# Optimization experiments

Hardware: AMD Instinct MI355X
Metric: run time of the kernel (lower is better)

Reference implementation:

```python
import jax, jax.numpy as jnp
import numpy as np

HEADS = 16
KEY_SIZE = 64
HEAD_SIZE = 64
D_MODEL = 1024
MASK_BIG = 1e12


def setup_inputs() -> dict:
    key = jax.random.key(0)
    ks = jax.random.split(key, 16)
    B, S, D = 4, 2048, D_MODEL
    qk_dim = HEADS * KEY_SIZE
    out_dim = HEADS * HEAD_SIZE
    s = 0.02
    return {
        'q': jax.random.normal(ks[0], (B, S, D), jnp.float32),
        'k': jax.random.normal(ks[1], (B, S, D), jnp.float32),
        'v': jax.random.normal(ks[2], (B, S, D), jnp.float32),
        'q_mask': jax.random.randint(ks[3], (B, S), 0, 2, jnp.int32),
        'v_mask': jax.random.randint(ks[4], (B, S), 0, 2, jnp.int32),
        'Wq': jax.random.normal(ks[5], (D, qk_dim), jnp.float32) * s,
        'bq': jnp.zeros((qk_dim,), jnp.float32),
        'Wk': jax.random.normal(ks[6], (D, qk_dim), jnp.float32) * s,
        'bk': jnp.zeros((qk_dim,), jnp.float32),
        'Wv': jax.random.normal(ks[7], (D, out_dim), jnp.float32) * s,
        'bv': jnp.zeros((out_dim,), jnp.float32),
        'Wo': jax.random.normal(ks[8], (out_dim, out_dim), jnp.float32) * s,
        'bo': jnp.zeros((out_dim,), jnp.float32),
    }


def reference(q, k, v, q_mask, v_mask, Wq, bq, Wk, bk, Wv, bv, Wo, bo):
    B, Sq, _ = q.shape
    Sk = k.shape[1]
    # projections -> [B, H, S, d]
    qw = (q @ Wq + bq).reshape(B, Sq, HEADS, KEY_SIZE).transpose(0, 2, 1, 3)
    kw = (k @ Wk + bk).reshape(B, Sk, HEADS, KEY_SIZE).transpose(0, 2, 1, 3)
    vw = (v @ Wv + bv).reshape(B, Sk, HEADS, HEAD_SIZE).transpose(0, 2, 1, 3)
    # scaled dot-product scores [B, H, Sq, Sk]
    a = jnp.einsum('bhqd,bhkd->bhqk', qw, kw) / np.sqrt(KEY_SIZE).astype(np.float32)
    # v_mask: additive -inf-like penalty on padded keys (mode=1, axis=-1)
    vm = v_mask.astype(a.dtype)[:, None, None, :]
    a = a - (1.0 - vm) * MASK_BIG
    # a_mask=True: causal mask (mask future positions)
    causal = jnp.tril(jnp.ones((Sq, Sk), a.dtype))
    a = a - (1.0 - causal) * MASK_BIG
    a = jax.nn.softmax(a, axis=-1)
    # attention output [B, Sq, H*head_size]
    o = jnp.einsum('bhqk,bhkd->bhqd', a, vw).transpose(0, 2, 1, 3).reshape(B, Sq, HEADS * HEAD_SIZE)
    o = o @ Wo + bo
    # q_mask: multiplicative zeroing of padded query outputs (mode=0, axis=1)
    o = o * q_mask.astype(o.dtype)[:, :, None]
    return o
```

## Files before the change

kernel.cpp:

```cpp
#include <hip/hip_runtime.h>
#include <hip/hip_bf16.h>

typedef __attribute__((ext_vector_type(8))) short v8s;
typedef __attribute__((ext_vector_type(4))) float v4f;
typedef __attribute__((ext_vector_type(16))) float v16f;
typedef __attribute__((ext_vector_type(4))) unsigned v4u;

#define S_LEN 2048
#define NB 4
#define NH 16
#define LOG2E 1.4426950408889634f
#define CMASK 1443109011456.0f
#define DEFER_THR 11.55f

__device__ __forceinline__ short f2bf(float f) {
    __hip_bfloat16 h = __float2bfloat16(f);
    union { __hip_bfloat16 h; short s; } u; u.h = h; return u.s;
}

__device__ __forceinline__ unsigned cvtpk(float lo, float hi) {
    unsigned r;
    asm("v_cvt_pk_bf16_f32 %0, %1, %2" : "=v"(r) : "v"(lo), "v"(hi));
    return r;
}

__device__ __forceinline__ int swz(int row, int col) {
    return (row * 128 + col) ^ ((row & 7) << 4);
}

__device__ __forceinline__ void async16(void* lds, const void* g) {
    __builtin_amdgcn_global_load_lds(
        (const __attribute__((address_space(1))) unsigned int*)g,
        (__attribute__((address_space(3))) unsigned int*)lds, 16, 0, 0);
}

#define MFMA16(a, b, c) __builtin_amdgcn_mfma_f32_16x16x32_bf16((a), (b), (c), 0, 0, 0)
#define MFMA32(a, b, c) __builtin_amdgcn_mfma_f32_32x32x16_bf16((a), (b), (c), 0, 0, 0)

__global__ __launch_bounds__(256) void convert_all(const float* __restrict__ q,
                                                   const float* __restrict__ k,
                                                   const float* __restrict__ v,
                                                   short* __restrict__ Xq,
                                                   short* __restrict__ Xk,
                                                   short* __restrict__ Xv,
                                                   float* __restrict__ outz) {
    if (blockIdx.y == 3) {
        size_t i = ((size_t)blockIdx.x * 256 + threadIdx.x) * 8;
        float4 z4 = {0.f, 0.f, 0.f, 0.f};
        *(float4*)(outz + i) = z4;
        *(float4*)(outz + i + 4) = z4;
        return;
    }
    const float* in = (blockIdx.y == 0) ? q : (blockIdx.y == 1) ? k : v;
    short* out = (blockIdx.y == 0) ? Xq : (blockIdx.y == 1) ? Xk : Xv;
    size_t i = ((size_t)blockIdx.x * 256 + threadIdx.x) * 8;
    float4 a = *(const float4*)(in + i);
    float4 b = *(const float4*)(in + i + 4);
    v8s o;
    o[0] = f2bf(a.x); o[1] = f2bf(a.y); o[2] = f2bf(a.z); o[3] = f2bf(a.w);
    o[4] = f2bf(b.x); o[5] = f2bf(b.y); o[6] = f2bf(b.z); o[7] = f2bf(b.w);
    *(v8s*)(out + i) = o;
}

__global__ __launch_bounds__(256) void build_pen(const int* __restrict__ vm,
                                                 short* __restrict__ penC) {
    int i = blockIdx.x * 256 + threadIdx.x;
    penC[i] = vm[i] ? (short)0 : f2bf(-CMASK);
}

__global__ __launch_bounds__(256) void compact_qmask(const int* __restrict__ qm,
                                                     int* __restrict__ idx,
                                                     int* __restrict__ nq) {
    const int b = blockIdx.x;
    const int* m = qm + b * S_LEN;
    int* ib = idx + b * S_LEN;
    __shared__ int cnt[256];
    const int t = threadIdx.x;
    int loc[8], c = 0;
#pragma unroll
    for (int i = 0; i < 8; ++i) { int s = t * 8 + i; if (m[s]) loc[c++] = s; }
    cnt[t] = c;
    __syncthreads();
    for (int d = 1; d < 256; d <<= 1) {
        int v = (t >= d) ? cnt[t - d] : 0;
        __syncthreads();
        cnt[t] += v;
        __syncthreads();
    }
    int off = cnt[t] - c;
    for (int i = 0; i < c; ++i) ib[off + i] = loc[i];
    if (t == 255) nq[b] = cnt[255];
}

__global__ __launch_bounds__(256) void transpose_all(const float* __restrict__ Wq,
                                                     const float* __restrict__ Wk,
                                                     const float* __restrict__ Wv,
                                                     const float* __restrict__ Wo,
                                                     short* __restrict__ WTq,
                                                     short* __restrict__ WTk,
                                                     short* __restrict__ WTv,
                                                     short* __restrict__ WTo) {
    const int z = blockIdx.z;
    const float* W = (z == 0) ? Wq : (z == 1) ? Wk : (z == 2) ? Wv : Wo;
    short* WT = (z == 0) ? WTq : (z == 1) ? WTk : (z == 2) ? WTv : WTo;
    __shared__ float tile[32][33];
    int k0 = blockIdx.x * 32, n0 = blockIdx.y * 32;
    int tx = threadIdx.x & 31, ty = threadIdx.x >> 5;
#pragma unroll
    for (int i = 0; i < 4; ++i)
        tile[ty + i * 8][tx] = W[(size_t)(k0 + ty + i * 8) * 1024 + n0 + tx];
    __syncthreads();
#pragma unroll
    for (int i = 0; i < 4; ++i)
        WT[(size_t)(n0 + ty + i * 8) * 1024 + k0 + tx] = f2bf(tile[tx][ty + i * 8]);
}

__global__ __launch_bounds__(256)
void proj_all(const short* __restrict__ Xk, const short* __restrict__ Xv,
              const short* __restrict__ Xq,
              const short* __restrict__ WTk, const short* __restrict__ WTv,
              const short* __restrict__ WTq,
              const float* __restrict__ bk, const float* __restrict__ bv,
              const float* __restrict__ bq,
              const int* __restrict__ idx, const int* __restrict__ nq,
              short* __restrict__ KF, short* __restrict__ VF,
              short* __restrict__ QW) {
    __shared__ short As[2][128 * 64];
    __shared__ short Bs[2][128 * 64];
    const int tid = threadIdx.x;
    const int l = tid & 63, w = tid >> 6;
    const int g = l >> 4, ql = l & 15;
    const int z = blockIdx.z;
    const int bid = blockIdx.x;
    const int y = (bid & 7) + 8 * (bid >> 6);
    const int n0 = ((bid >> 3) & 7) * 128;
    const int wr = w >> 1, wc = w & 1;

    int b = 0, m0 = y * 128, m0c = 0, nqv = 0;
    const int* idxb = nullptr;
    if (z == 2) {
        if (y >= 36) return;
        b = y / 9; m0c = (y % 9) * 128;
        nqv = nq[b];
        if (m0c >= nqv) return;
        idxb = idx + b * S_LEN;
    }
    const short* A  = (z == 0) ? Xk : (z == 1) ? Xv : Xq;
    const short* BT = (z == 0) ? WTk : (z == 1) ? WTv : WTq;
    const float* bias = (z == 0) ? bk : (z == 1) ? bv : bq;

    int arow[4];
#pragma unroll
    for (int i = 0; i < 4; ++i) {
        int row = (i * 256 + tid) >> 3;
        if (z == 2) {
            int jc = m0c + row;
            arow[i] = b * S_LEN + idxb[(jc < nqv) ? jc : (nqv - 1)];
        } else {
            arow[i] = m0 + row;
        }
    }
    const int c8 = (((l & 7) ^ (l >> 3))) * 8;

    v4f acc[4][4] = {};

    auto stage = [&](int kt, int buf) {
        const int kk = kt * 64;
#pragma unroll
        for (int i = 0; i < 4; ++i) {
            int ci = i * 256 + tid;
            async16((char*)As[buf] + (size_t)(i * 256 + w * 64) * 16,
                    A + (size_t)arow[i] * 1024 + kk + c8);
            async16((char*)Bs[buf] + (size_t)(i * 256 + w * 64) * 16,
                    BT + (size_t)(n0 + (ci >> 3)) * 1024 + kk + c8);
        }
    };

    stage(0, 0);
    for (int kt = 0; kt < 16; ++kt) {
        __builtin_amdgcn_s_barrier();
        __builtin_amdgcn_sched_barrier(0);
        if (kt + 1 < 16) {
            stage(kt + 1, (kt + 1) & 1);
            asm volatile("s_waitcnt vmcnt(8)" ::: "memory");
        } else {
            asm volatile("s_waitcnt vmcnt(0)" ::: "memory");
        }
        __builtin_amdgcn_sched_barrier(0);
        __builtin_amdgcn_s_barrier();
        __builtin_amdgcn_sched_barrier(0);
        const short* Ab = As[kt & 1];
        const short* Bb = Bs[kt & 1];
#pragma unroll
        for (int ks = 0; ks < 2; ++ks) {
            v8s af[4], bfr[4];
#pragma unroll
            for (int mt = 0; mt < 4; ++mt)
                af[mt] = *(const v8s*)((char*)Ab +
                          swz(wr * 64 + mt * 16 + ql, ks * 64 + g * 16));
#pragma unroll
            for (int nt = 0; nt < 4; ++nt)
                bfr[nt] = *(const v8s*)((char*)Bb +
                          swz(wc * 64 + nt * 16 + ql, ks * 64 + g * 16));
#pragma unroll
            for (int mt = 0; mt < 4; ++mt)
#pragma unroll
                for (int nt = 0; nt < 4; ++nt)
                    acc[mt][nt] = MFMA16(af[mt], bfr[nt], acc[mt][nt]);
        }
    }

#pragma unroll
    for (int nt = 0; nt < 4; ++nt) {
        int col = n0 + wc * 64 + nt * 16 + ql;
        float bval = bias[col];
        int hh = col >> 6, dd = col & 63;
#pragma unroll
        for (int mt = 0; mt < 4; ++mt) {
#pragma unroll
            for (int r = 0; r < 4; ++r) {
                int lrow = wr * 64 + mt * 16 + g * 4 + r;
                float vv = acc[mt][nt][r] + bval;
                if (z == 0) {
                    int gm = m0 + lrow;
                    int bb = gm >> 11, ss = gm & 2047;
                    size_t base = (size_t)(bb * NH + hh) * 131072
                                + (size_t)(ss >> 6) * 4096
                                + (dd >> 4) * 1024 + (ss & 63) * 16
                                + ((dd >> 3) & 1) * 8 + (dd & 7);
                    KF[base] = f2bf(vv);
                } else if (z == 1) {
                    int gm = m0 + lrow;
                    int bb = gm >> 11, ss = gm & 2047;
                    int wkp = ss & 63;
                    size_t base = (size_t)(bb * NH + hh) * 131072
                                + (size_t)(ss >> 6) * 4096
                                + (wkp >> 4) * 1024 + dd * 16
                                + ((wkp >> 3) & 1) * 8 + (wkp & 7);
                    VF[base] = f2bf(vv);
                } else {
                    int jc = m0c + lrow;
                    vv *= 0.125f * LOG2E;
                    QW[((size_t)(b * NH + hh) * S_LEN + jc) * 64 + dd] = f2bf(vv);
                }
            }
        }
    }
}

__global__ __launch_bounds__(64)
void attn_kernel(const short* __restrict__ QW, const short* __restrict__ KF,
                 const short* __restrict__ VF, const short* __restrict__ penC,
                 const int* __restrict__ idx, const int* __restrict__ nq,
                 short* __restrict__ O) {
    const int l = threadIdx.x;
    const int lq = l & 31, hi = l >> 5;
    const int bh = blockIdx.x;
    const int chunk = 63 - (int)blockIdx.y;
    const int b = bh >> 4, hd = bh & 15;

    const int nqv = nq[b];
    const int cy = chunk * 32;
    if (cy >= nqv) return;

    const short* Qp = QW + (size_t)bh * S_LEN * 64;
    const short* Kp = KF + (size_t)bh * 131072;
    const short* Vp = VF + (size_t)bh * 131072;
    const short* pp = penC + b * S_LEN;
    const int* idxb = idx + b * S_LEN;

    const int j = cy + lq;
    const int jj = (j < nqv) ? j : (nqv - 1);
    const int q_glob = idxb[jj];
    const int qmin = __builtin_amdgcn_readfirstlane(q_glob);

    int lastj = cy + 31; if (lastj > nqv - 1) lastj = nqv - 1;
    const int NT = (idxb[lastj] >> 6) + 1;

    v8s qf[4];
#pragma unroll
    for (int ks = 0; ks < 4; ++ks)
        qf[ks] = *(const v8s*)(Qp + (size_t)jj * 64 + ks * 16 + hi * 8);
    v8s qf4 = {};
    qf4[0] = hi ? (short)0 : (short)0x3F80;

    v16f accO[2] = {};
    float m_run = -INFINITY, l_run = 0.f;

    auto tile = [&](int kt, bool causal) {
        const int k0 = kt * 64;
        const short* Kt = Kp + (size_t)kt * 4096;
        const short* Vt = Vp + (size_t)kt * 4096;
        short p0 = pp[k0 + lq], p1 = pp[k0 + lq + 32];

        v8s kf0[4], kf1[4];
#pragma unroll
        for (int ks = 0; ks < 4; ++ks) {
            kf0[ks] = *(const v8s*)(Kt + ks * 1024 + lq * 16 + hi * 8);
            kf1[ks] = *(const v8s*)(Kt + ks * 1024 + (lq + 32) * 16 + hi * 8);
        }
        v16f acc0 = {}, acc1 = {};
        __builtin_amdgcn_s_setprio(1);
#pragma unroll
        for (int ks = 0; ks < 4; ++ks) {
            acc0 = MFMA32(kf0[ks], qf[ks], acc0);
            acc1 = MFMA32(kf1[ks], qf[ks], acc1);
        }
        v8s k4a = {}, k4b = {};
        k4a[0] = hi ? (short)0 : p0;
        k4b[0] = hi ? (short)0 : p1;
        acc0 = MFMA32(k4a, qf4, acc0);
        acc1 = MFMA32(k4b, qf4, acc1);
        __builtin_amdgcn_s_setprio(0);

        float s[32];
#pragma unroll
        for (int jn = 0; jn < 16; ++jn) { s[jn] = acc0[jn]; s[16 + jn] = acc1[jn]; }
        if (causal) {
#pragma unroll
            for (int t = 0; t < 2; ++t)
#pragma unroll
                for (int jn = 0; jn < 16; ++jn) {
                    int kp = k0 + t * 32 + (jn & 3) + 8 * (jn >> 2) + 4 * hi;
                    if (kp > q_glob) s[t * 16 + jn] -= CMASK;
                }
        }
        float t8[8];
#pragma unroll
        for (int i = 0; i < 8; ++i)
            t8[i] = fmaxf(fmaxf(s[i], s[i + 8]), fmaxf(s[i + 16], s[i + 24]));
#pragma unroll
        for (int i = 0; i < 4; ++i) t8[i] = fmaxf(t8[i], t8[i + 4]);
        float tmax = fmaxf(fmaxf(t8[0], t8[1]), fmaxf(t8[2], t8[3]));
        tmax = fmaxf(tmax, __shfl_xor(tmax, 32, 64));

        if (__any(tmax > m_run + DEFER_THR)) {
            float mnew = fmaxf(m_run, tmax);
            float scale = exp2f(m_run - mnew);
            m_run = mnew;
            l_run *= scale;
#pragma unroll
            for (int jn = 0; jn < 16; ++jn) {
                float sc = __shfl(scale, (jn & 3) + 8 * (jn >> 2) + 4 * hi, 64);
                accO[0][jn] *= sc;
                accO[1][jn] *= sc;
            }
        }
#pragma unroll
        for (int i = 0; i < 32; ++i) s[i] = exp2f(s[i] - m_run);
        float u8[8];
#pragma unroll
        for (int i = 0; i < 8; ++i)
            u8[i] = (s[i] + s[i + 8]) + (s[i + 16] + s[i + 24]);
#pragma unroll
        for (int i = 0; i < 4; ++i) u8[i] += u8[i + 4];
        float psum = (u8[0] + u8[1]) + (u8[2] + u8[3]);
        psum += __shfl_xor(psum, 32, 64);
        l_run += psum;

        v8s vf0[4], vf1[4];
#pragma unroll
        for (int ks = 0; ks < 4; ++ks) {
            vf0[ks] = *(const v8s*)(Vt + ks * 1024 + lq * 16 + hi * 8);
            vf1[ks] = *(const v8s*)(Vt + ks * 1024 + (lq + 32) * 16 + hi * 8);
        }

        v8s PA[4];
#pragma unroll
        for (int t = 0; t < 2; ++t)
#pragma unroll
            for (int sf = 0; sf < 2; ++sf) {
                int base = t * 16 + sf * 8;
                unsigned x0 = cvtpk(s[base + 0], s[base + 1]);
                unsigned x1 = cvtpk(s[base + 2], s[base + 3]);
                unsigned y0 = cvtpk(s[base + 4], s[base + 5]);
                unsigned y1 = cvtpk(s[base + 6], s[base + 7]);
                asm volatile("v_permlane32_swap_b32 %0, %1" : "+v"(x0), "+v"(y0));
                asm volatile("v_permlane32_swap_b32 %0, %1" : "+v"(x1), "+v"(y1));
                v4u wv; wv[0] = x0; wv[1] = x1; wv[2] = y0; wv[3] = y1;
                union { v4u u; v8s s8; } cvt; cvt.u = wv;
                PA[t * 2 + sf] = cvt.s8;
            }

        __builtin_amdgcn_s_setprio(1);
#pragma unroll
        for (int ks = 0; ks < 4; ++ks) {
            accO[0] = MFMA32(PA[ks], vf0[ks], accO[0]);
            accO[1] = MFMA32(PA[ks], vf1[ks], accO[1]);
        }
        __builtin_amdgcn_s_setprio(0);
    };

    for (int kt = 0; kt < NT; ++kt)
        tile(kt, kt * 64 + 63 > qmin);

    int kt = NT;
    while (kt < 32 && __any(m_run < -1e11f)) {
        tile(kt, true);
        ++kt;
    }

    float inv = 1.0f / l_run;
#pragma unroll
    for (int jn = 0; jn < 16; ++jn) {
        int rowq = (jn & 3) + 8 * (jn >> 2) + 4 * hi;
        float iv = __shfl(inv, rowq, 64);
        int jrow = cy + rowq;
        if (jrow < nqv) {
            size_t base = (size_t)(b * S_LEN + jrow) * 1024 + hd * 64 + lq;
            O[base]      = f2bf(accO[0][jn] * iv);
            O[base + 32] = f2bf(accO[1][jn] * iv);
        }
    }
}

__global__ __launch_bounds__(256)
void out_gemm_c(const short* __restrict__ A, const short* __restrict__ BT,
                const float* __restrict__ bias, const int* __restrict__ idx,
                const int* __restrict__ nq, float* __restrict__ out) {
    __shared__ short As[2][128 * 64];
    __shared__ short Bs[2][128 * 64];
    const int tid = threadIdx.x;
    const int l = tid & 63, w = tid >> 6;
    const int g = l >> 4, ql = l & 15;
    const int bid = blockIdx.x;
    const int y = (bid & 7) + 8 * (bid >> 6);
    if (y >= 36) return;
    const int n0 = ((bid >> 3) & 7) * 128;
    const int b = y / 9;
    const int m0c = (y % 9) * 128;
    const int nqv = nq[b];
    if (m0c >= nqv) return;
    const int* idxb = idx + b * S_LEN;
    const int wr = w >> 1, wc = w & 1;
    const int c8 = (((l & 7) ^ (l >> 3))) * 8;

    v4f acc[4][4] = {};

    auto stage = [&](int kt, int buf) {
        const int kk = kt * 64;
#pragma unroll
        for (int i = 0; i < 4; ++i) {
            int ci = i * 256 + tid;
            int row = ci >> 3;
            async16((char*)As[buf] + (size_t)(i * 256 + w * 64) * 16,
                    A + (size_t)(b * S_LEN + m0c + row) * 1024 + kk + c8);
            async16((char*)Bs[buf] + (size_t)(i * 256 + w * 64) * 16,
                    BT + (size_t)(n0 + row) * 1024 + kk + c8);
        }
    };

    stage(0, 0);
    for (int kt = 0; kt < 16; ++kt) {
        __builtin_amdgcn_s_barrier();
        __builtin_amdgcn_sched_barrier(0);
        if (kt + 1 < 16) {
            stage(kt + 1, (kt + 1) & 1);
            asm volatile("s_waitcnt vmcnt(8)" ::: "memory");
        } else {
            asm volatile("s_waitcnt vmcnt(0)" ::: "memory");
        }
        __builtin_amdgcn_sched_barrier(0);
        __builtin_amdgcn_s_barrier();
        __builtin_amdgcn_sched_barrier(0);
        const short* Ab = As[kt & 1];
        const short* Bb = Bs[kt & 1];
#pragma unroll
        for (int ks = 0; ks < 2; ++ks) {
            v8s af[4], bfr[4];
#pragma unroll
            for (int mt = 0; mt < 4; ++mt)
                af[mt] = *(const v8s*)((char*)Ab +
                          swz(wr * 64 + mt * 16 + ql, ks * 64 + g * 16));
#pragma unroll
            for (int nt = 0; nt < 4; ++nt)
                bfr[nt] = *(const v8s*)((char*)Bb +
                          swz(wc * 64 + nt * 16 + ql, ks * 64 + g * 16));
#pragma unroll
            for (int mt = 0; mt < 4; ++mt)
#pragma unroll
                for (int nt = 0; nt < 4; ++nt)
                    acc[mt][nt] = MFMA16(af[mt], bfr[nt], acc[mt][nt]);
        }
    }

#pragma unroll
    for (int nt = 0; nt < 4; ++nt) {
        int col = n0 + wc * 64 + nt * 16 + ql;
        float bval = bias[col];
#pragma unroll
        for (int mt = 0; mt < 4; ++mt) {
#pragma unroll
            for (int r = 0; r < 4; ++r) {
                int jc = m0c + wr * 64 + mt * 16 + g * 4 + r;
                if (jc < nqv) {
                    int orig = idxb[jc];
                    out[(size_t)(b * S_LEN + orig) * 1024 + col] =
                        acc[mt][nt][r] + bval;
                }
            }
        }
    }
}

extern "C" void kernel_launch(void* const* d_in, const int* in_sizes, int n_in,
                              void* d_out, int out_size, void* d_ws, size_t ws_size,
                              hipStream_t stream) {
    (void)in_sizes; (void)n_in; (void)out_size; (void)ws_size;
    const float* q  = (const float*)d_in[0];
    const float* k  = (const float*)d_in[1];
    const float* v  = (const float*)d_in[2];
    const int* qmask = (const int*)d_in[3];
    const int* vmask = (const int*)d_in[4];
    const float* Wq = (const float*)d_in[5];
    const float* bq = (const float*)d_in[6];
    const float* Wk = (const float*)d_in[7];
    const float* bk = (const float*)d_in[8];
    const float* Wv = (const float*)d_in[9];
    const float* bv = (const float*)d_in[10];
    const float* Wo = (const float*)d_in[11];
    const float* bo = (const float*)d_in[12];
    float* out = (float*)d_out;

    char* ws = (char*)d_ws;
    const size_t MB = 1024 * 1024;
    short* Xq  = (short*)(ws + 0 * MB);
    short* Xk  = (short*)(ws + 16 * MB);
    short* Xv  = (short*)(ws + 32 * MB);
    short* WTq = (short*)(ws + 48 * MB);
    short* WTk = (short*)(ws + 50 * MB);
    short* WTv = (short*)(ws + 52 * MB);
    short* WTo = (short*)(ws + 54 * MB);
    short* QW  = (short*)(ws + 56 * MB);
    short* KF  = (short*)(ws + 72 * MB);
    short* VFb = (short*)(ws + 88 * MB);
    short* Ob  = (short*)(ws + 104 * MB);
    short* penC = (short*)(ws + 120 * MB);
    int* idxB  = (int*)(ws + 121 * MB);
    int* nqB   = (int*)(ws + 122 * MB);

    convert_all<<<dim3(4096, 4), 256, 0, stream>>>(q, k, v, Xq, Xk, Xv, out);
    transpose_all<<<dim3(32, 32, 4), 256, 0, stream>>>(Wq, Wk, Wv, Wo,
                                                       WTq, WTk, WTv, WTo);
    build_pen<<<32, 256, 0, stream>>>(vmask, penC);
    compact_qmask<<<NB, 256, 0, stream>>>(qmask, idxB, nqB);

    proj_all<<<dim3(512, 1, 3), 256, 0, stream>>>(Xk, Xv, Xq, WTk, WTv, WTq,
                                                  bk, bv, bq, idxB, nqB,
                                                  KF, VFb, QW);
    attn_kernel<<<dim3(64, 64), 64, 0, stream>>>(QW, KF, VFb, penC, idxB, nqB, Ob);
    out_gemm_c<<<320, 256, 0, stream>>>(Ob, WTo, bo, idxB, nqB, out);
}
```

Before: 219.9 us.

## Fuse fp32-to-bf16 input conversion into projection GEMM A-tile staging

Removes the separate convert pass that turned q, k and v into bf16 scratch buffers. The projection kernel now loads fp32 activations straight into registers, packs them to bf16 and writes them into swizzled LDS, double-buffering across two register sets. Output zeroing moves to its own small kernel. This avoids writing and re-reading about 48MB of bf16 intermediates, at the cost of more register pressure, doubled A-tile global reads per GEMM iteration, and synchronous LDS writes in the main loop.

```diff
diff --git a/kernel.cpp b/kernel.cpp
--- a/kernel.cpp
+++ b/kernel.cpp
@@ -37,29 +37,11 @@
 #define MFMA16(a, b, c) __builtin_amdgcn_mfma_f32_16x16x32_bf16((a), (b), (c), 0, 0, 0)
 #define MFMA32(a, b, c) __builtin_amdgcn_mfma_f32_32x32x16_bf16((a), (b), (c), 0, 0, 0)
 
-__global__ __launch_bounds__(256) void convert_all(const float* __restrict__ q,
-                                                   const float* __restrict__ k,
-                                                   const float* __restrict__ v,
-                                                   short* __restrict__ Xq,
-                                                   short* __restrict__ Xk,
-                                                   short* __restrict__ Xv,
-                                                   float* __restrict__ outz) {
-    if (blockIdx.y == 3) {
-        size_t i = ((size_t)blockIdx.x * 256 + threadIdx.x) * 8;
-        float4 z4 = {0.f, 0.f, 0.f, 0.f};
-        *(float4*)(outz + i) = z4;
-        *(float4*)(outz + i + 4) = z4;
-        return;
-    }
-    const float* in = (blockIdx.y == 0) ? q : (blockIdx.y == 1) ? k : v;
-    short* out = (blockIdx.y == 0) ? Xq : (blockIdx.y == 1) ? Xk : Xv;
-    size_t i = ((size_t)blockIdx.x * 256 + threadIdx.x) * 8;
-    float4 a = *(const float4*)(in + i);
-    float4 b = *(const float4*)(in + i + 4);
-    v8s o;
-    o[0] = f2bf(a.x); o[1] = f2bf(a.y); o[2] = f2bf(a.z); o[3] = f2bf(a.w);
-    o[4] = f2bf(b.x); o[5] = f2bf(b.y); o[6] = f2bf(b.z); o[7] = f2bf(b.w);
-    *(v8s*)(out + i) = o;
+__global__ __launch_bounds__(256) void zero_out(float* __restrict__ out) {
+    size_t i = ((size_t)blockIdx.x * 256 + threadIdx.x) * 16;
+    float4 z = {0.f, 0.f, 0.f, 0.f};
+#pragma unroll
+    for (int k = 0; k < 4; ++k) *(float4*)(out + i + k * 4) = z;
 }
 
 __global__ __launch_bounds__(256) void build_pen(const int* __restrict__ vm,
@@ -116,8 +98,8 @@
 }
 
 __global__ __launch_bounds__(256)
-void proj_all(const short* __restrict__ Xk, const short* __restrict__ Xv,
-              const short* __restrict__ Xq,
+void proj_all(const float* __restrict__ kI, const float* __restrict__ vI,
+              const float* __restrict__ qI,
               const short* __restrict__ WTk, const short* __restrict__ WTv,
               const short* __restrict__ WTq,
               const float* __restrict__ bk, const float* __restrict__ bv,
@@ -145,7 +127,7 @@
         if (m0c >= nqv) return;
         idxb = idx + b * S_LEN;
     }
-    const short* A  = (z == 0) ? Xk : (z == 1) ? Xv : Xq;
+    const float* Af = (z == 0) ? kI : (z == 1) ? vI : qI;
     const short* BT = (z == 0) ? WTk : (z == 1) ? WTv : WTq;
     const float* bias = (z == 0) ? bk : (z == 1) ? bv : bq;
 
@@ -160,32 +142,61 @@
             arow[i] = m0 + row;
         }
     }
-    const int c8 = (((l & 7) ^ (l >> 3))) * 8;
+    const int c8  = (((l & 7) ^ (l >> 3))) * 8;
+    const int c8a = (tid & 7) * 8;
 
     v4f acc[4][4] = {};
-
-    auto stage = [&](int kt, int buf) {
+    float4 f4A[8], f4B[8];
+
+    auto issueB = [&](int kt, int buf) {
         const int kk = kt * 64;
 #pragma unroll
         for (int i = 0; i < 4; ++i) {
             int ci = i * 256 + tid;
-            async16((char*)As[buf] + (size_t)(i * 256 + w * 64) * 16,
-                    A + (size_t)arow[i] * 1024 + kk + c8);
-            async16((char*)Bs[buf] + (size_t)(i * 256 + w * 64) * 16,
+            async16((char*)Bs[buf] + (size_t)ci * 16,
                     BT + (size_t)(n0 + (ci >> 3)) * 1024 + kk + c8);
         }
     };
-
-    stage(0, 0);
+    auto issueA = [&](int kt, float4* fr) {
+        const int kk = kt * 64;
+#pragma unroll
+        for (int i = 0; i < 4; ++i) {
+            const float* src = Af + (size_t)arow[i] * 1024 + kk + c8a;
+            fr[2 * i]     = *(const float4*)(src);
+            fr[2 * i + 1] = *(const float4*)(src + 4);
+        }
+    };
+    auto writeA = [&](int buf, const float4* fr) {
+#pragma unroll
+        for (int i = 0; i < 4; ++i) {
+            int ci = i * 256 + tid;
+            int row = ci >> 3;
+            v4u wv;
+            wv[0] = cvtpk(fr[2 * i].x, fr[2 * i].y);
+            wv[1] = cvtpk(fr[2 * i].z, fr[2 * i].w);
+            wv[2] = cvtpk(fr[2 * i + 1].x, fr[2 * i + 1].y);
+            wv[3] = cvtpk(fr[2 * i + 1].z, fr[2 * i + 1].w);
+            *(v4u*)((char*)As[buf] + swz(row, (tid & 7) * 16)) = wv;
+        }
+    };
+
+    issueB(0, 0);
+    issueA(0, f4A);
     for (int kt = 0; kt < 16; ++kt) {
         __builtin_amdgcn_s_barrier();
         __builtin_amdgcn_sched_barrier(0);
         if (kt + 1 < 16) {
-            stage(kt + 1, (kt + 1) & 1);
-            asm volatile("s_waitcnt vmcnt(8)" ::: "memory");
+            issueB(kt + 1, (kt + 1) & 1);
+            if (kt & 1) issueA(kt + 1, f4A);
+            else        issueA(kt + 1, f4B);
+            asm volatile("s_waitcnt vmcnt(12)" ::: "memory");
         } else {
             asm volatile("s_waitcnt vmcnt(0)" ::: "memory");
         }
+        __builtin_amdgcn_sched_barrier(0);
+        if (kt & 1) writeA(1, f4B);
+        else        writeA(0, f4A);
+        asm volatile("s_waitcnt lgkmcnt(0)" ::: "memory");
         __builtin_amdgcn_sched_barrier(0);
         __builtin_amdgcn_s_barrier();
         __builtin_amdgcn_sched_barrier(0);
@@ -524,9 +535,6 @@
 
     char* ws = (char*)d_ws;
     const size_t MB = 1024 * 1024;
-    short* Xq  = (short*)(ws + 0 * MB);
-    short* Xk  = (short*)(ws + 16 * MB);
-    short* Xv  = (short*)(ws + 32 * MB);
     short* WTq = (short*)(ws + 48 * MB);
     short* WTk = (short*)(ws + 50 * MB);
     short* WTv = (short*)(ws + 52 * MB);
@@ -539,13 +547,13 @@
     int* idxB  = (int*)(ws + 121 * MB);
     int* nqB   = (int*)(ws + 122 * MB);
 
-    convert_all<<<dim3(4096, 4), 256, 0, stream>>>(q, k, v, Xq, Xk, Xv, out);
     transpose_all<<<dim3(32, 32, 4), 256, 0, stream>>>(Wq, Wk, Wv, Wo,
                                                        WTq, WTk, WTv, WTo);
     build_pen<<<32, 256, 0, stream>>>(vmask, penC);
     compact_qmask<<<NB, 256, 0, stream>>>(qmask, idxB, nqB);
-
-    proj_all<<<dim3(512, 1, 3), 256, 0, stream>>>(Xk, Xv, Xq, WTk, WTv, WTq,
+    zero_out<<<2048, 256, 0, stream>>>(out);
+
+    proj_all<<<dim3(512, 1, 3), 256, 0, stream>>>(k, v, q, WTk, WTv, WTq,
                                                   bk, bv, bq, idxB, nqB,
                                                   KF, VFb, QW);
     attn_kernel<<<dim3(64, 64), 64, 0, stream>>>(QW, KF, VFb, penC, idxB, nqB, Ob);
```

New measurement: 226.4 us. 2.9% more time.
